# Kernel optimization log

Measured on AMD Instinct MI355X. Metric: run time of the kernel, lower is better.

Reference implementation:

```python
import jax, jax.numpy as jnp
import numpy as np

DIM = 256
NUM_HEADS = 8
HEAD_DIM = DIM // NUM_HEADS
WS = 7                 # window_size
N = WS * WS            # tokens per window
B = 4096               # batch * num_windows


def _make_rel_index(ws):
    coords = np.stack(np.meshgrid(np.arange(ws), np.arange(ws), indexing='ij'))  # [2,ws,ws]
    cf = coords.reshape(2, -1)                                                   # [2,N]
    rel = cf[:, :, None] - cf[:, None, :]                                        # [2,N,N]
    rel = rel.transpose(1, 2, 0).copy()
    rel[:, :, 0] += ws - 1
    rel[:, :, 1] += ws - 1
    rel[:, :, 0] *= 2 * ws - 1
    return rel.sum(-1).astype(np.int32)                                          # [N,N]


def setup_inputs() -> dict:
    key = jax.random.key(0)
    ks = jax.random.split(key, 6)
    x = jax.random.normal(ks[0], (B, N, DIM), dtype=jnp.float32)
    qkv_w = jax.random.normal(ks[1], (3 * DIM, DIM), dtype=jnp.float32) * 0.02
    qkv_b = jax.random.normal(ks[2], (3 * DIM,), dtype=jnp.float32) * 0.02
    proj_w = jax.random.normal(ks[3], (DIM, DIM), dtype=jnp.float32) * 0.02
    proj_b = jax.random.normal(ks[4], (DIM,), dtype=jnp.float32) * 0.02
    bias_table = jax.random.normal(ks[5], ((2 * WS - 1) ** 2, NUM_HEADS), dtype=jnp.float32) * 0.02
    rel_index = jnp.asarray(_make_rel_index(WS))
    return {"x": x, "qkv_w": qkv_w, "qkv_b": qkv_b, "proj_w": proj_w,
            "proj_b": proj_b, "bias_table": bias_table, "rel_index": rel_index}


def reference(x, qkv_w, qkv_b, proj_w, proj_b, bias_table, rel_index):
    B_, n, C = x.shape
    scale = HEAD_DIM ** (-0.5)
    # qkv projection -> [3, B, H, N, hd]
    qkv = (x @ qkv_w.T + qkv_b).reshape(B_, n, 3, NUM_HEADS, HEAD_DIM)
    qkv = qkv.transpose(2, 0, 3, 1, 4)
    q, k, v = qkv[0], qkv[1], qkv[2]
    attn = jnp.einsum('bhnd,bhmd->bhnm', q * scale, k)
    # relative position bias gather: [N,N,H] -> [1,H,N,N]
    rel_bias = bias_table[rel_index]                       # [N,N,H]
    attn = attn + rel_bias.transpose(2, 0, 1)[None]
    attn = jax.nn.softmax(attn, axis=-1)
    out = jnp.einsum('bhnm,bhmd->bhnd', attn, v)           # [B,H,N,hd]
    out = out.transpose(0, 2, 1, 3).reshape(B_, n, C)
    return out @ proj_w.T + proj_b
```

## Files before the change

kernel.cpp:

```cpp
#include <hip/hip_runtime.h>
#include <hip/hip_bf16.h>
#include <stdint.h>

#define NWIN 4096

typedef __attribute__((ext_vector_type(8))) short bf16x8;
typedef __attribute__((ext_vector_type(4))) float f32x4;

#define OFF_WQ 0LL
#define OFF_WP 393216LL
#define OFF_RB 524288LL
#define OFF_B  655360LL

static __device__ __forceinline__ uint32_t f2bf(float f) {
    union { float f; uint32_t u; } v; v.f = f;
    return (v.u + 0x7FFFu + ((v.u >> 16) & 1u)) >> 16;
}

static __device__ __forceinline__ uint32_t pk2(float lo, float hi) {
    union { __hip_bfloat162 h; uint32_t u; } c;
    c.h = __float22bfloat162_rn(float2{lo, hi});
    return c.u;
}

static __device__ __forceinline__ int permd(int p) {
    return ((p >> 2) & 3) * 8 + (p >> 4) * 4 + (p & 3);
}

union FragU { uint32_t u[4]; bf16x8 v; };

__global__ void prep_kernel(const float* __restrict__ qkv_w, const float* __restrict__ proj_w,
                            const float* __restrict__ qkv_b,
                            const float* __restrict__ bias_table, const int* __restrict__ rel_index,
                            char* __restrict__ ws) {
    uint16_t* wq  = (uint16_t*)(ws + OFF_WQ);
    uint16_t* wp  = (uint16_t*)(ws + OFF_WP);
    float*    rb  = (float*)(ws + OFF_RB);
    float*    wsb = (float*)(ws + OFF_B);
    const int total = 196608 + 65536 + 32768 + 768;
    for (int idx = blockIdx.x * blockDim.x + threadIdx.x; idx < total;
         idx += gridDim.x * blockDim.x) {
        if (idx < 196608) {
            int n = idx >> 8, c = idx & 255;
            int src = (n < 512) ? ((n & ~31) | permd(n & 31)) : n;
            wq[idx] = (uint16_t)f2bf(qkv_w[src * 256 + c]);
        } else if (idx < 262144) {
            int i = idx - 196608;
            wp[i] = (uint16_t)f2bf(proj_w[i]);
        } else if (idx < 294912) {
            int i = idx - 262144;
            int h = i >> 12, kt4 = (i >> 8) & 15, qt = (i >> 2) & 63, ii = i & 3;
            int kt = kt4 * 4 + ii;
            float v = -1e30f;
            if (kt < 49 && qt < 49)
                v = bias_table[rel_index[qt * 49 + kt] * 8 + h] * 1.4426950408889634f;
            rb[i] = v;
        } else {
            int n = idx - 294912;
            int src = (n < 512) ? ((n & ~31) | permd(n & 31)) : n;
            wsb[n] = qkv_b[src];
        }
    }
}

__global__ __launch_bounds__(512, 2) void fused_kernel(const float* __restrict__ x,
                                                       const float* __restrict__ proj_b,
                                                       float* __restrict__ out,
                                                       const char* __restrict__ ws) {
    __shared__ __align__(16) char smem[33792];
    const int b = blockIdx.x;
    const int t = threadIdx.x, lane = t & 63, w = t >> 6;
    const int lr = lane & 15, lg = lane >> 4;
    const uint16_t* wq  = (const uint16_t*)(ws + OFF_WQ);
    const uint16_t* wp  = (const uint16_t*)(ws + OFF_WP);
    const float*    rb  = (const float*)(ws + OFF_RB);
    const float*    wsb = (const float*)(ws + OFF_B);
    uint16_t* X  = (uint16_t*)smem;
    char*     OL = smem;
    const float scale = 0.17677669529663687f * 1.4426950408889634f;

    {
        const float4* xv = (const float4*)x;
        #pragma unroll
        for (int it = 0; it < 8; ++it) {
            int idx = it * 512 + t;
            int row = idx >> 6, c4 = idx & 63;
            uint32_t lo = 0, hi = 0;
            if (row < 49) {
                float4 v4 = xv[((int64_t)b * 49 + row) * 64 + c4];
                lo = pk2(v4.x, v4.y);
                hi = pk2(v4.z, v4.w);
            }
            uint32_t* p = (uint32_t*)(X + row * 264 + c4 * 4);
            p[0] = lo; p[1] = hi;
        }
    }
    __syncthreads();

    bf16x8 qf[4], kf[4];
    {
        f32x4 aq[2][4], ak[2][4];
        #pragma unroll
        for (int mt = 0; mt < 2; ++mt)
            #pragma unroll
            for (int t4 = 0; t4 < 4; ++t4) {
                aq[mt][t4] = (f32x4){0.f, 0.f, 0.f, 0.f};
                ak[mt][t4] = (f32x4){0.f, 0.f, 0.f, 0.f};
            }
        #pragma unroll
        for (int kk = 0; kk < 8; ++kk) {
            bf16x8 xf[4];
            #pragma unroll
            for (int t4 = 0; t4 < 4; ++t4)
                xf[t4] = *(const bf16x8*)(X + (16 * t4 + lr) * 264 + kk * 32 + lg * 8);
            #pragma unroll
            for (int mt = 0; mt < 2; ++mt) {
                bf16x8 wfq = *(const bf16x8*)(wq + (w * 32 + 16 * mt + lr) * 256 + kk * 32 + lg * 8);
                bf16x8 wfk = *(const bf16x8*)(wq + (256 + w * 32 + 16 * mt + lr) * 256 + kk * 32 + lg * 8);
                #pragma unroll
                for (int t4 = 0; t4 < 4; ++t4) {
                    aq[mt][t4] = __builtin_amdgcn_mfma_f32_16x16x32_bf16(wfq, xf[t4], aq[mt][t4], 0, 0, 0);
                    ak[mt][t4] = __builtin_amdgcn_mfma_f32_16x16x32_bf16(wfk, xf[t4], ak[mt][t4], 0, 0, 0);
                }
            }
        }
        f32x4 bq[2], bk[2];
        #pragma unroll
        for (int mt = 0; mt < 2; ++mt) {
            bq[mt] = *(const f32x4*)(wsb + w * 32 + 16 * mt + 4 * lg);
            bk[mt] = *(const f32x4*)(wsb + 256 + w * 32 + 16 * mt + 4 * lg);
        }
        #pragma unroll
        for (int t4 = 0; t4 < 4; ++t4) {
            FragU q, k;
            #pragma unroll
            for (int mt = 0; mt < 2; ++mt) {
                q.u[2 * mt]     = pk2(aq[mt][t4][0] + bq[mt][0], aq[mt][t4][1] + bq[mt][1]);
                q.u[2 * mt + 1] = pk2(aq[mt][t4][2] + bq[mt][2], aq[mt][t4][3] + bq[mt][3]);
                k.u[2 * mt]     = pk2(ak[mt][t4][0] + bk[mt][0], ak[mt][t4][1] + bk[mt][1]);
                k.u[2 * mt + 1] = pk2(ak[mt][t4][2] + bk[mt][2], ak[mt][t4][3] + bk[mt][3]);
            }
            qf[t4] = q.v; kf[t4] = k.v;
        }
    }

    float rs[4];
    bf16x8 pf[4][2];
    #pragma unroll
    for (int nj = 0; nj < 4; ++nj) {
        f32x4 s[4];
        __builtin_amdgcn_s_setprio(1);
        #pragma unroll
        for (int mj = 0; mj < 4; ++mj)
            s[mj] = __builtin_amdgcn_mfma_f32_16x16x32_bf16(
                kf[mj], qf[nj], (f32x4){0.f, 0.f, 0.f, 0.f}, 0, 0, 0);
        __builtin_amdgcn_s_setprio(0);
        #pragma unroll
        for (int mj = 0; mj < 4; ++mj) {
            f32x4 rbv = *(const f32x4*)(rb + ((w * 16 + 4 * mj + lg) * 64 + 16 * nj + lr) * 4);
            s[mj] = s[mj] * scale + rbv;
        }
        float m = s[0][0];
        #pragma unroll
        for (int mj = 0; mj < 4; ++mj)
            #pragma unroll
            for (int i = 0; i < 4; ++i) m = fmaxf(m, s[mj][i]);
        m = fmaxf(m, __shfl_xor(m, 16));
        m = fmaxf(m, __shfl_xor(m, 32));
        float sum = 0.f;
        #pragma unroll
        for (int mj = 0; mj < 4; ++mj)
            #pragma unroll
            for (int i = 0; i < 4; ++i) {
                float e = __builtin_amdgcn_exp2f(s[mj][i] - m);
                s[mj][i] = e;
                sum += e;
            }
        sum += __shfl_xor(sum, 16);
        sum += __shfl_xor(sum, 32);
        rs[nj] = sum;
        #pragma unroll
        for (int ks = 0; ks < 2; ++ks) {
            FragU f;
            f.u[0] = pk2(s[2 * ks][0], s[2 * ks][1]);
            f.u[1] = pk2(s[2 * ks][2], s[2 * ks][3]);
            f.u[2] = pk2(s[2 * ks + 1][0], s[2 * ks + 1][1]);
            f.u[3] = pk2(s[2 * ks + 1][2], s[2 * ks + 1][3]);
            pf[nj][ks] = f.v;
        }
    }

    __builtin_amdgcn_sched_barrier(0);

    bf16x8 vf[2][2];
    {
        f32x4 av[4][2];
        #pragma unroll
        for (int t4 = 0; t4 < 4; ++t4)
            #pragma unroll
            for (int dn = 0; dn < 2; ++dn)
                av[t4][dn] = (f32x4){0.f, 0.f, 0.f, 0.f};
        #pragma unroll
        for (int kk = 0; kk < 8; ++kk) {
            bf16x8 xf[4];
            #pragma unroll
            for (int t4 = 0; t4 < 4; ++t4)
                xf[t4] = *(const bf16x8*)(X + (16 * t4 + lr) * 264 + kk * 32 + lg * 8);
            #pragma unroll
            for (int dn = 0; dn < 2; ++dn) {
                bf16x8 wf = *(const bf16x8*)(wq + (512 + w * 32 + 16 * dn + lr) * 256 + kk * 32 + lg * 8);
                #pragma unroll
                for (int t4 = 0; t4 < 4; ++t4)
                    av[t4][dn] = __builtin_amdgcn_mfma_f32_16x16x32_bf16(xf[t4], wf, av[t4][dn], 0, 0, 0);
            }
        }
        #pragma unroll
        for (int dt = 0; dt < 2; ++dt) {
            const float bv = wsb[512 + w * 32 + 16 * dt + lr];
            #pragma unroll
            for (int ks = 0; ks < 2; ++ks) {
                FragU f;
                f.u[0] = pk2(av[2 * ks][dt][0] + bv, av[2 * ks][dt][1] + bv);
                f.u[1] = pk2(av[2 * ks][dt][2] + bv, av[2 * ks][dt][3] + bv);
                f.u[2] = pk2(av[2 * ks + 1][dt][0] + bv, av[2 * ks + 1][dt][1] + bv);
                f.u[3] = pk2(av[2 * ks + 1][dt][2] + bv, av[2 * ks + 1][dt][3] + bv);
                vf[dt][ks] = f.v;
            }
        }
    }

    f32x4 o[2][4];
    __builtin_amdgcn_s_setprio(1);
    #pragma unroll
    for (int dt = 0; dt < 2; ++dt)
        #pragma unroll
        for (int nj = 0; nj < 4; ++nj) {
            f32x4 acc = __builtin_amdgcn_mfma_f32_16x16x32_bf16(
                vf[dt][0], pf[nj][0], (f32x4){0.f, 0.f, 0.f, 0.f}, 0, 0, 0);
            o[dt][nj] = __builtin_amdgcn_mfma_f32_16x16x32_bf16(vf[dt][1], pf[nj][1], acc, 0, 0, 0);
        }
    __builtin_amdgcn_s_setprio(0);

    __syncthreads();
    #pragma unroll
    for (int nj = 0; nj < 4; ++nj) {
        const float rinv = 1.0f / rs[nj];
        const int row = 16 * nj + lr;
        const int swz = (row & 7) << 4;
        #pragma unroll
        for (int dt = 0; dt < 2; ++dt) {
            uint2 pk;
            pk.x = pk2(o[dt][nj][0] * rinv, o[dt][nj][1] * rinv);
            pk.y = pk2(o[dt][nj][2] * rinv, o[dt][nj][3] * rinv);
            *(uint2*)(OL + ((row * 512 + w * 64 + dt * 32 + lg * 8) ^ swz)) = pk;
        }
    }
    __syncthreads();

    f32x4 pacc[4][2];
    #pragma unroll
    for (int mi = 0; mi < 4; ++mi)
        #pragma unroll
        for (int nj = 0; nj < 2; ++nj)
            pacc[mi][nj] = (f32x4){0.f, 0.f, 0.f, 0.f};
    #pragma unroll
    for (int kk = 0; kk < 8; ++kk) {
        bf16x8 av[4];
        #pragma unroll
        for (int mi = 0; mi < 4; ++mi) {
            const int row = mi * 16 + lr;
            av[mi] = *(const bf16x8*)(OL + ((row * 512 + kk * 64 + lg * 16) ^ ((row & 7) << 4)));
        }
        #pragma unroll
        for (int nj = 0; nj < 2; ++nj) {
            bf16x8 bv = *(const bf16x8*)(wp + (w * 32 + nj * 16 + lr) * 256 + kk * 32 + lg * 8);
            #pragma unroll
            for (int mi = 0; mi < 4; ++mi)
                pacc[mi][nj] = __builtin_amdgcn_mfma_f32_16x16x32_bf16(av[mi], bv, pacc[mi][nj], 0, 0, 0);
        }
    }
    #pragma unroll
    for (int nj = 0; nj < 2; ++nj) {
        const int n = w * 32 + nj * 16 + lr;
        const float pb = proj_b[n];
        #pragma unroll
        for (int mi = 0; mi < 4; ++mi)
            #pragma unroll
            for (int i = 0; i < 4; ++i) {
                const int tok = mi * 16 + lg * 4 + i;
                if (tok < 49)
                    out[((int64_t)b * 49 + tok) * 256 + n] = pacc[mi][nj][i] + pb;
            }
    }
}

extern "C" void kernel_launch(void* const* d_in, const int* in_sizes, int n_in,
                              void* d_out, int out_size, void* d_ws, size_t ws_size,
                              hipStream_t stream) {
    const float* x          = (const float*)d_in[0];
    const float* qkv_w      = (const float*)d_in[1];
    const float* qkv_b      = (const float*)d_in[2];
    const float* proj_w     = (const float*)d_in[3];
    const float* proj_b     = (const float*)d_in[4];
    const float* bias_table = (const float*)d_in[5];
    const int*   rel_index  = (const int*)d_in[6];
    float* out = (float*)d_out;
    char*  ws  = (char*)d_ws;

    prep_kernel<<<1155, 256, 0, stream>>>(qkv_w, proj_w, qkv_b, bias_table, rel_index, ws);
    fused_kernel<<<NWIN, 512, 0, stream>>>(x, proj_b, out, ws);
}
```

Before: 369.7 us.

## Split fused window attention into separate QKV GEMM, attention, and projection kernels

Replaces the single per-window fused kernel with three kernels: a tiled 128x128 bf16 GEMM for the QKV projection that writes Q/K/V per head to workspace, a per-window attention kernel that reads those tensors, and a tiled GEMM for the output projection. The aim is better weight reuse and no padding waste from 49-token windows in the GEMMs, since the old kernel reloaded the full weight matrices from global memory for every window. The cost is extra global-memory round trips for bf16 Q/K/V and the attention output (hundreds of MB of workspace traffic) plus additional launches.

```diff
diff --git a/kernel.cpp b/kernel.cpp
--- a/kernel.cpp
+++ b/kernel.cpp
@@ -11,6 +11,10 @@
 #define OFF_WP 393216LL
 #define OFF_RB 524288LL
 #define OFF_B  655360LL
+#define OFF_Q  1048576LL
+#define QKV_STRIDE 102760448LL
+#define OFF_K  (OFF_Q + QKV_STRIDE)
+#define OFF_V  (OFF_Q + 2 * QKV_STRIDE)
 
 static __device__ __forceinline__ uint32_t f2bf(float f) {
     union { float f; uint32_t u; } v; v.f = f;
@@ -21,10 +25,6 @@
     union { __hip_bfloat162 h; uint32_t u; } c;
     c.h = __float22bfloat162_rn(float2{lo, hi});
     return c.u;
-}
-
-static __device__ __forceinline__ int permd(int p) {
-    return ((p >> 2) & 3) * 8 + (p >> 4) * 4 + (p & 3);
 }
 
 union FragU { uint32_t u[4]; bf16x8 v; };
@@ -41,9 +41,7 @@
     for (int idx = blockIdx.x * blockDim.x + threadIdx.x; idx < total;
          idx += gridDim.x * blockDim.x) {
         if (idx < 196608) {
-            int n = idx >> 8, c = idx & 255;
-            int src = (n < 512) ? ((n & ~31) | permd(n & 31)) : n;
-            wq[idx] = (uint16_t)f2bf(qkv_w[src * 256 + c]);
+            wq[idx] = (uint16_t)f2bf(qkv_w[idx]);
         } else if (idx < 262144) {
             int i = idx - 196608;
             wp[i] = (uint16_t)f2bf(proj_w[i]);
@@ -57,92 +55,135 @@
             rb[i] = v;
         } else {
             int n = idx - 294912;
-            int src = (n < 512) ? ((n & ~31) | permd(n & 31)) : n;
-            wsb[n] = qkv_b[src];
-        }
-    }
-}
-
-__global__ __launch_bounds__(512, 2) void fused_kernel(const float* __restrict__ x,
-                                                       const float* __restrict__ proj_b,
-                                                       float* __restrict__ out,
-                                                       const char* __restrict__ ws) {
-    __shared__ __align__(16) char smem[33792];
+            wsb[n] = qkv_b[n];
+        }
+    }
+}
+
+__global__ __launch_bounds__(256, 2) void qkv_kernel(const float* __restrict__ x,
+                                                     char* __restrict__ ws) {
+    __shared__ __align__(16) char smem[32768];
+    uint16_t* A  = (uint16_t*)smem;
+    uint16_t* Bt = (uint16_t*)(smem + 16384);
+    const uint16_t* wq  = (const uint16_t*)(ws + OFF_WQ);
+    const float*    wsb = (const float*)(ws + OFF_B);
+    const int m0 = blockIdx.x * 128, n0 = blockIdx.y * 128;
+    const int t = threadIdx.x, l = t & 63, w = t >> 6;
+    const int lr = l & 15, lg = l >> 4;
+    const int wm = w >> 1, wn = w & 1;
+    f32x4 acc[4][4];
+    #pragma unroll
+    for (int a = 0; a < 4; ++a)
+        #pragma unroll
+        for (int b2 = 0; b2 < 4; ++b2) acc[a][b2] = (f32x4){0.f, 0.f, 0.f, 0.f};
+
+    for (int kk = 0; kk < 4; ++kk) {
+        #pragma unroll
+        for (int it = 0; it < 4; ++it) {
+            int item = it * 256 + t;
+            int r = item >> 3, ch = item & 7;
+            const float* src = x + (int64_t)(m0 + r) * 256 + kk * 64 + ch * 8;
+            float4 v0 = *(const float4*)src;
+            float4 v1 = *(const float4*)(src + 4);
+            uint4 pk;
+            pk.x = pk2(v0.x, v0.y); pk.y = pk2(v0.z, v0.w);
+            pk.z = pk2(v1.x, v1.y); pk.w = pk2(v1.z, v1.w);
+            *(uint4*)((char*)A + ((r * 128 + ch * 16) ^ ((r & 7) << 4))) = pk;
+        }
+        #pragma unroll
+        for (int it = 0; it < 4; ++it) {
+            int item = it * 256 + t;
+            int r = item >> 3, ch = item & 7;
+            uint4 v = *(const uint4*)(wq + (int64_t)(n0 + r) * 256 + kk * 64 + ch * 8);
+            *(uint4*)((char*)Bt + ((r * 128 + ch * 16) ^ ((r & 7) << 4))) = v;
+        }
+        __syncthreads();
+        #pragma unroll
+        for (int kh = 0; kh < 2; ++kh) {
+            bf16x8 af[4], bfr[4];
+            #pragma unroll
+            for (int mi = 0; mi < 4; ++mi) {
+                int r = wm * 64 + 16 * mi + lr;
+                af[mi] = *(const bf16x8*)((char*)A + ((r * 128 + kh * 64 + lg * 16) ^ ((r & 7) << 4)));
+            }
+            #pragma unroll
+            for (int nj = 0; nj < 4; ++nj) {
+                int r = wn * 64 + 16 * nj + lr;
+                bfr[nj] = *(const bf16x8*)((char*)Bt + ((r * 128 + kh * 64 + lg * 16) ^ ((r & 7) << 4)));
+            }
+            #pragma unroll
+            for (int nj = 0; nj < 4; ++nj)
+                #pragma unroll
+                for (int mi = 0; mi < 4; ++mi)
+                    acc[nj][mi] = __builtin_amdgcn_mfma_f32_16x16x32_bf16(bfr[nj], af[mi], acc[nj][mi], 0, 0, 0);
+        }
+        __syncthreads();
+    }
+    uint16_t* C = (uint16_t*)smem;
+    #pragma unroll
+    for (int nj = 0; nj < 4; ++nj) {
+        f32x4 bias = *(const f32x4*)(wsb + n0 + wn * 64 + 16 * nj + 4 * lg);
+        #pragma unroll
+        for (int mi = 0; mi < 4; ++mi) {
+            int tok_l = wm * 64 + 16 * mi + lr;
+            int nb = wn * 64 + 16 * nj + 4 * lg;
+            uint2 pk;
+            pk.x = pk2(acc[nj][mi][0] + bias[0], acc[nj][mi][1] + bias[1]);
+            pk.y = pk2(acc[nj][mi][2] + bias[2], acc[nj][mi][3] + bias[3]);
+            *(uint2*)((char*)C + ((tok_l * 256 + nb * 2) ^ ((tok_l & 7) << 4))) = pk;
+        }
+    }
+    __syncthreads();
+    const int sel = n0 >> 8;
+    char* dstBase = ws + OFF_Q + (int64_t)sel * QKV_STRIDE;
+    #pragma unroll
+    for (int it = 0; it < 8; ++it) {
+        int hh = it >> 1;
+        int mrow = ((it & 1) << 6) | (t >> 2);
+        int q4 = t & 3;
+        uint4 v = *(const uint4*)((char*)C + ((mrow * 256 + hh * 64 + q4 * 16) ^ ((mrow & 7) << 4)));
+        int m = m0 + mrow;
+        int b = m / 49;
+        int tok = m - b * 49;
+        int h = ((n0 >> 5) + hh) & 7;
+        *(uint4*)(dstBase + (((int64_t)b * 8 + h) * 49 + tok) * 64 + q4 * 16) = v;
+    }
+}
+
+__global__ __launch_bounds__(512, 2) void attn_kernel(char* __restrict__ ws) {
+    __shared__ __align__(16) char smem[32768];
     const int b = blockIdx.x;
-    const int t = threadIdx.x, lane = t & 63, w = t >> 6;
-    const int lr = lane & 15, lg = lane >> 4;
-    const uint16_t* wq  = (const uint16_t*)(ws + OFF_WQ);
-    const uint16_t* wp  = (const uint16_t*)(ws + OFF_WP);
-    const float*    rb  = (const float*)(ws + OFF_RB);
-    const float*    wsb = (const float*)(ws + OFF_B);
-    uint16_t* X  = (uint16_t*)smem;
-    char*     OL = smem;
+    const int t = threadIdx.x, l = t & 63, w = t >> 6;
+    const int lr = l & 15, lg = l >> 4;
+    const uint16_t* Q = (const uint16_t*)(ws + OFF_Q);
+    const uint16_t* K = (const uint16_t*)(ws + OFF_K);
+    const uint16_t* V = (const uint16_t*)(ws + OFF_V);
+    const float*   rb = (const float*)(ws + OFF_RB);
+    char* VL = smem + w * 4096;
+    char* OL = smem;
     const float scale = 0.17677669529663687f * 1.4426950408889634f;
-
-    {
-        const float4* xv = (const float4*)x;
-        #pragma unroll
-        for (int it = 0; it < 8; ++it) {
-            int idx = it * 512 + t;
-            int row = idx >> 6, c4 = idx & 63;
-            uint32_t lo = 0, hi = 0;
-            if (row < 49) {
-                float4 v4 = xv[((int64_t)b * 49 + row) * 64 + c4];
-                lo = pk2(v4.x, v4.y);
-                hi = pk2(v4.z, v4.w);
-            }
-            uint32_t* p = (uint32_t*)(X + row * 264 + c4 * 4);
-            p[0] = lo; p[1] = hi;
-        }
-    }
-    __syncthreads();
+    const int64_t bh = (int64_t)b * 8 + w;
+
+    uint4 vstage[4];
+    int   vc[4];
+    #pragma unroll
+    for (int it = 0; it < 4; ++it) {
+        int item = it * 64 + l;
+        int tok = item >> 2, d0 = (item & 3) * 8;
+        int a = tok >> 4, g = (tok >> 2) & 3, ii = tok & 3;
+        vc[it] = (a >> 1) * 32 + g * 8 + (a & 1) * 4 + ii;
+        uint4 v = {0u, 0u, 0u, 0u};
+        if (tok < 49) v = *(const uint4*)(V + (bh * 49 + tok) * 32 + d0);
+        vstage[it] = v;
+    }
 
     bf16x8 qf[4], kf[4];
-    {
-        f32x4 aq[2][4], ak[2][4];
-        #pragma unroll
-        for (int mt = 0; mt < 2; ++mt)
-            #pragma unroll
-            for (int t4 = 0; t4 < 4; ++t4) {
-                aq[mt][t4] = (f32x4){0.f, 0.f, 0.f, 0.f};
-                ak[mt][t4] = (f32x4){0.f, 0.f, 0.f, 0.f};
-            }
-        #pragma unroll
-        for (int kk = 0; kk < 8; ++kk) {
-            bf16x8 xf[4];
-            #pragma unroll
-            for (int t4 = 0; t4 < 4; ++t4)
-                xf[t4] = *(const bf16x8*)(X + (16 * t4 + lr) * 264 + kk * 32 + lg * 8);
-            #pragma unroll
-            for (int mt = 0; mt < 2; ++mt) {
-                bf16x8 wfq = *(const bf16x8*)(wq + (w * 32 + 16 * mt + lr) * 256 + kk * 32 + lg * 8);
-                bf16x8 wfk = *(const bf16x8*)(wq + (256 + w * 32 + 16 * mt + lr) * 256 + kk * 32 + lg * 8);
-                #pragma unroll
-                for (int t4 = 0; t4 < 4; ++t4) {
-                    aq[mt][t4] = __builtin_amdgcn_mfma_f32_16x16x32_bf16(wfq, xf[t4], aq[mt][t4], 0, 0, 0);
-                    ak[mt][t4] = __builtin_amdgcn_mfma_f32_16x16x32_bf16(wfk, xf[t4], ak[mt][t4], 0, 0, 0);
-                }
-            }
-        }
-        f32x4 bq[2], bk[2];
-        #pragma unroll
-        for (int mt = 0; mt < 2; ++mt) {
-            bq[mt] = *(const f32x4*)(wsb + w * 32 + 16 * mt + 4 * lg);
-            bk[mt] = *(const f32x4*)(wsb + 256 + w * 32 + 16 * mt + 4 * lg);
-        }
-        #pragma unroll
-        for (int t4 = 0; t4 < 4; ++t4) {
-            FragU q, k;
-            #pragma unroll
-            for (int mt = 0; mt < 2; ++mt) {
-                q.u[2 * mt]     = pk2(aq[mt][t4][0] + bq[mt][0], aq[mt][t4][1] + bq[mt][1]);
-                q.u[2 * mt + 1] = pk2(aq[mt][t4][2] + bq[mt][2], aq[mt][t4][3] + bq[mt][3]);
-                k.u[2 * mt]     = pk2(ak[mt][t4][0] + bk[mt][0], ak[mt][t4][1] + bk[mt][1]);
-                k.u[2 * mt + 1] = pk2(ak[mt][t4][2] + bk[mt][2], ak[mt][t4][3] + bk[mt][3]);
-            }
-            qf[t4] = q.v; kf[t4] = k.v;
-        }
-    }
+    #pragma unroll
+    for (int nj = 0; nj < 4; ++nj)
+        qf[nj] = *(const bf16x8*)(Q + (bh * 49 + 16 * nj + lr) * 32 + lg * 8);
+    #pragma unroll
+    for (int mj = 0; mj < 4; ++mj)
+        kf[mj] = *(const bf16x8*)(K + (bh * 49 + 16 * mj + lr) * 32 + lg * 8);
 
     float rs[4];
     bf16x8 pf[4][2];
@@ -190,44 +231,27 @@
         }
     }
 
-    __builtin_amdgcn_sched_barrier(0);
-
+    #pragma unroll
+    for (int it = 0; it < 4; ++it) {
+        int item = it * 64 + l;
+        int d0 = (item & 3) * 8;
+        int c = vc[it];
+        const uint32_t words[4] = {vstage[it].x, vstage[it].y, vstage[it].z, vstage[it].w};
+        #pragma unroll
+        for (int jj = 0; jj < 4; ++jj) {
+            int dA = d0 + 2 * jj, dB = dA + 1;
+            *(uint16_t*)(VL + ((dA * 128 + c * 2) ^ ((dA & 7) << 4))) = (uint16_t)words[jj];
+            *(uint16_t*)(VL + ((dB * 128 + c * 2) ^ ((dB & 7) << 4))) = (uint16_t)(words[jj] >> 16);
+        }
+    }
     bf16x8 vf[2][2];
-    {
-        f32x4 av[4][2];
-        #pragma unroll
-        for (int t4 = 0; t4 < 4; ++t4)
-            #pragma unroll
-            for (int dn = 0; dn < 2; ++dn)
-                av[t4][dn] = (f32x4){0.f, 0.f, 0.f, 0.f};
-        #pragma unroll
-        for (int kk = 0; kk < 8; ++kk) {
-            bf16x8 xf[4];
-            #pragma unroll
-            for (int t4 = 0; t4 < 4; ++t4)
-                xf[t4] = *(const bf16x8*)(X + (16 * t4 + lr) * 264 + kk * 32 + lg * 8);
-            #pragma unroll
-            for (int dn = 0; dn < 2; ++dn) {
-                bf16x8 wf = *(const bf16x8*)(wq + (512 + w * 32 + 16 * dn + lr) * 256 + kk * 32 + lg * 8);
-                #pragma unroll
-                for (int t4 = 0; t4 < 4; ++t4)
-                    av[t4][dn] = __builtin_amdgcn_mfma_f32_16x16x32_bf16(xf[t4], wf, av[t4][dn], 0, 0, 0);
-            }
-        }
-        #pragma unroll
-        for (int dt = 0; dt < 2; ++dt) {
-            const float bv = wsb[512 + w * 32 + 16 * dt + lr];
-            #pragma unroll
-            for (int ks = 0; ks < 2; ++ks) {
-                FragU f;
-                f.u[0] = pk2(av[2 * ks][dt][0] + bv, av[2 * ks][dt][1] + bv);
-                f.u[1] = pk2(av[2 * ks][dt][2] + bv, av[2 * ks][dt][3] + bv);
-                f.u[2] = pk2(av[2 * ks + 1][dt][0] + bv, av[2 * ks + 1][dt][1] + bv);
-                f.u[3] = pk2(av[2 * ks + 1][dt][2] + bv, av[2 * ks + 1][dt][3] + bv);
-                vf[dt][ks] = f.v;
-            }
-        }
-    }
+    #pragma unroll
+    for (int dt = 0; dt < 2; ++dt)
+        #pragma unroll
+        for (int ks = 0; ks < 2; ++ks) {
+            int row = dt * 16 + lr;
+            vf[dt][ks] = *(const bf16x8*)(VL + ((row * 128 + ks * 64 + lg * 16) ^ ((row & 7) << 4)));
+        }
 
     f32x4 o[2][4];
     __builtin_amdgcn_s_setprio(1);
@@ -256,41 +280,86 @@
         }
     }
     __syncthreads();
-
-    f32x4 pacc[4][2];
-    #pragma unroll
-    for (int mi = 0; mi < 4; ++mi)
-        #pragma unroll
-        for (int nj = 0; nj < 2; ++nj)
-            pacc[mi][nj] = (f32x4){0.f, 0.f, 0.f, 0.f};
-    #pragma unroll
-    for (int kk = 0; kk < 8; ++kk) {
-        bf16x8 av[4];
+    char* OWS = ws + OFF_V;
+    #pragma unroll
+    for (int it = 0; it < 4; ++it) {
+        int c = it * 512 + t;
+        if (c < 1568) {
+            int tok = c >> 5, ch = c & 31;
+            uint4 v = *(const uint4*)(OL + ((tok * 512 + ch * 16) ^ ((tok & 7) << 4)));
+            *(uint4*)(OWS + ((int64_t)b * 49 + tok) * 512 + ch * 16) = v;
+        }
+    }
+}
+
+__global__ __launch_bounds__(256, 2) void proj_kernel(const float* __restrict__ proj_b,
+                                                      float* __restrict__ out,
+                                                      const char* __restrict__ ws) {
+    __shared__ __align__(16) char smem[65536];
+    uint16_t* A  = (uint16_t*)smem;
+    uint16_t* Bt = (uint16_t*)(smem + 16384);
+    const uint16_t* OWS = (const uint16_t*)(ws + OFF_V);
+    const uint16_t* wp  = (const uint16_t*)(ws + OFF_WP);
+    const int m0 = blockIdx.x * 128, n0 = blockIdx.y * 128;
+    const int t = threadIdx.x, l = t & 63, w = t >> 6;
+    const int lr = l & 15, lg = l >> 4;
+    const int wm = w >> 1, wn = w & 1;
+    f32x4 acc[4][4];
+    #pragma unroll
+    for (int a = 0; a < 4; ++a)
+        #pragma unroll
+        for (int b2 = 0; b2 < 4; ++b2) acc[a][b2] = (f32x4){0.f, 0.f, 0.f, 0.f};
+
+    for (int kk = 0; kk < 4; ++kk) {
+        #pragma unroll
+        for (int it = 0; it < 4; ++it) {
+            int item = it * 256 + t;
+            int r = item >> 3, ch = item & 7;
+            uint4 va = *(const uint4*)(OWS + (int64_t)(m0 + r) * 256 + kk * 64 + ch * 8);
+            *(uint4*)((char*)A + ((r * 128 + ch * 16) ^ ((r & 7) << 4))) = va;
+            uint4 vb = *(const uint4*)(wp + (int64_t)(n0 + r) * 256 + kk * 64 + ch * 8);
+            *(uint4*)((char*)Bt + ((r * 128 + ch * 16) ^ ((r & 7) << 4))) = vb;
+        }
+        __syncthreads();
+        #pragma unroll
+        for (int kh = 0; kh < 2; ++kh) {
+            bf16x8 af[4], bfr[4];
+            #pragma unroll
+            for (int mi = 0; mi < 4; ++mi) {
+                int r = wm * 64 + 16 * mi + lr;
+                af[mi] = *(const bf16x8*)((char*)A + ((r * 128 + kh * 64 + lg * 16) ^ ((r & 7) << 4)));
+            }
+            #pragma unroll
+            for (int nj = 0; nj < 4; ++nj) {
+                int r = wn * 64 + 16 * nj + lr;
+                bfr[nj] = *(const bf16x8*)((char*)Bt + ((r * 128 + kh * 64 + lg * 16) ^ ((r & 7) << 4)));
+            }
+            #pragma unroll
+            for (int nj = 0; nj < 4; ++nj)
+                #pragma unroll
+                for (int mi = 0; mi < 4; ++mi)
+                    acc[nj][mi] = __builtin_amdgcn_mfma_f32_16x16x32_bf16(bfr[nj], af[mi], acc[nj][mi], 0, 0, 0);
+        }
+        __syncthreads();
+    }
+    float* C = (float*)smem;
+    #pragma unroll
+    for (int nj = 0; nj < 4; ++nj)
         #pragma unroll
         for (int mi = 0; mi < 4; ++mi) {
-            const int row = mi * 16 + lr;
-            av[mi] = *(const bf16x8*)(OL + ((row * 512 + kk * 64 + lg * 16) ^ ((row & 7) << 4)));
-        }
-        #pragma unroll
-        for (int nj = 0; nj < 2; ++nj) {
-            bf16x8 bv = *(const bf16x8*)(wp + (w * 32 + nj * 16 + lr) * 256 + kk * 32 + lg * 8);
-            #pragma unroll
-            for (int mi = 0; mi < 4; ++mi)
-                pacc[mi][nj] = __builtin_amdgcn_mfma_f32_16x16x32_bf16(av[mi], bv, pacc[mi][nj], 0, 0, 0);
-        }
-    }
-    #pragma unroll
-    for (int nj = 0; nj < 2; ++nj) {
-        const int n = w * 32 + nj * 16 + lr;
-        const float pb = proj_b[n];
-        #pragma unroll
-        for (int mi = 0; mi < 4; ++mi)
-            #pragma unroll
-            for (int i = 0; i < 4; ++i) {
-                const int tok = mi * 16 + lg * 4 + i;
-                if (tok < 49)
-                    out[((int64_t)b * 49 + tok) * 256 + n] = pacc[mi][nj][i] + pb;
-            }
+            int tok_l = wm * 64 + 16 * mi + lr;
+            int nb = wn * 64 + 16 * nj + 4 * lg;
+            *(f32x4*)((char*)C + ((tok_l * 512 + nb * 4) ^ ((tok_l & 7) << 4))) = acc[nj][mi];
+        }
+    __syncthreads();
+    #pragma unroll
+    for (int it = 0; it < 16; ++it) {
+        int c = it * 256 + t;
+        int mrow = c >> 5, ch = c & 31;
+        f32x4 v = *(const f32x4*)((char*)C + ((mrow * 512 + ch * 16) ^ ((mrow & 7) << 4)));
+        f32x4 bias = *(const f32x4*)(proj_b + n0 + ch * 4);
+        v = v + bias;
+        *(f32x4*)(out + (int64_t)(m0 + mrow) * 256 + n0 + ch * 4) = v;
     }
 }
 
@@ -308,5 +377,7 @@
     char*  ws  = (char*)d_ws;
 
     prep_kernel<<<1155, 256, 0, stream>>>(qkv_w, proj_w, qkv_b, bias_table, rel_index, ws);
-    fused_kernel<<<NWIN, 512, 0, stream>>>(x, proj_b, out, ws);
-}
+    qkv_kernel<<<dim3(1568, 6), 256, 0, stream>>>(x, ws);
+    attn_kernel<<<NWIN, 512, 0, stream>>>(ws);
+    proj_kernel<<<dim3(1568, 2), 256, 0, stream>>>(proj_b, out, ws);
+}
```

Result: slower. 404.0 us (+9.3%).
